# Kernel tuning notes

Measured on AMD Instinct MI355X. Metric: run time of the kernel, lower is better.

Reference implementation:

```python
import jax, jax.numpy as jnp
import numpy as np

N = 1024
H = 128

def setup_inputs() -> dict:
    key = jax.random.key(0)
    ks = jax.random.split(key, 16)
    s = 1.0 / np.sqrt(H)
    inp = {
        "h": jax.random.normal(ks[0], (N, H), jnp.float32),
        "x": jax.random.normal(ks[1], (N, 2), jnp.float32),
        "batch": jnp.zeros((N,), jnp.int64),
        # Linear params stored as [in, out]
        "Wq": jax.random.normal(ks[2], (H, H), jnp.float32) * s,
        "bq": jnp.zeros((H,), jnp.float32),
        "Wk": jax.random.normal(ks[3], (H, H), jnp.float32) * s,
        "bk": jnp.zeros((H,), jnp.float32),
        "Wv": jax.random.normal(ks[4], (H, H), jnp.float32) * s,
        "bv": jnp.zeros((H,), jnp.float32),
        "We1": jax.random.normal(ks[5], (2, H), jnp.float32) * (1.0 / np.sqrt(2.0)),
        "be1": jnp.zeros((H,), jnp.float32),
        "We2": jax.random.normal(ks[6], (H, H), jnp.float32) * s,
        "be2": jnp.zeros((H,), jnp.float32),
        "Wc": jax.random.normal(ks[7], (H, 1), jnp.float32) * s,
        "bc": jnp.zeros((1,), jnp.float32),
    }
    return inp

def reference(h, x, batch, Wq, bq, Wk, bk, Wv, bv, We1, be1, We2, be2, Wc, bc):
    hidden = h.shape[-1]
    # pairwise relative coordinates: [N, N, 2]
    rel_x = x[:, None, :] - x[None, :, :]
    # edge MLP: Linear(2->H) -> ReLU -> Linear(H->H), [N, N, H]
    edge_feat = jax.nn.relu(rel_x @ We1 + be1) @ We2 + be2
    # attention: scaled dot-product over all pairs
    q = h @ Wq + bq
    k = h @ Wk + bk
    v = h @ Wv + bv
    attn_score = (q @ k.T) / jnp.sqrt(jnp.asarray(hidden, h.dtype))  # [N, N]
    attn_weight = jax.nn.softmax(attn_score, axis=-1)
    agg_h = attn_weight @ v  # [N, H]
    # coordinate update: per-pair scalar gate times rel_x, attn-weighted sum over j
    gate = edge_feat @ Wc + bc                     # [N, N, 1]
    delta_x = jnp.sum(attn_weight[:, :, None] * gate * rel_x, axis=1)  # [N, 2]
    return (h + agg_h, x + delta_x)
```

## Files before the change

### kernel.cpp

```cpp
#include <hip/hip_runtime.h>
#include <math.h>

#define NN 1024
#define HH 128

typedef _Float16 h2 __attribute__((ext_vector_type(2)));
typedef _Float16 h4 __attribute__((ext_vector_type(4)));

__device__ inline float fdot2(h2 a, h2 b, float c) {
  return __builtin_amdgcn_fdot2(a, b, c, false);
}

__global__ __launch_bounds__(384) void qkv_kernel(
    const float* __restrict__ h,
    const float* __restrict__ Wq, const float* __restrict__ bq,
    const float* __restrict__ Wk, const float* __restrict__ bk,
    const float* __restrict__ Wv, const float* __restrict__ bv,
    const float* __restrict__ We2, const float* __restrict__ be2,
    const float* __restrict__ Wc, const float* __restrict__ bc,
    float* __restrict__ q, h2* __restrict__ kTp, h2* __restrict__ vp,
    float* __restrict__ Wc2, float* __restrict__ bc2) {
  const int t = threadIdx.x;

  if (blockIdx.x == 256) {
    if (t < HH) {
      float a = 0.f;
      for (int d = 0; d < HH; ++d) a = fmaf(We2[t * HH + d], Wc[d], a);
      Wc2[t] = a;
      if (t == 0) {
        float b = bc[0];
        for (int d = 0; d < HH; ++d) b = fmaf(be2[d], Wc[d], b);
        *bc2 = b;
      }
    }
    return;
  }

  __shared__ float4 hs4[HH];
  const int r0 = blockIdx.x * 4;
  if (t < HH) {
    hs4[t] = make_float4(h[(r0 + 0) * HH + t], h[(r0 + 1) * HH + t],
                         h[(r0 + 2) * HH + t], h[(r0 + 3) * HH + t]);
  }
  __syncthreads();

  const int mat = t >> 7;
  const int col = t & 127;
  const float* W = (mat == 0) ? Wq : (mat == 1) ? Wk : Wv;
  const float* B = (mat == 0) ? bq : (mat == 1) ? bk : bv;
  const float b = B[col];
  float a0 = b, a1 = b, a2 = b, a3 = b;
#pragma unroll 8
  for (int c = 0; c < HH; ++c) {
    float w = W[c * HH + col];
    float4 hv = hs4[c];
    a0 = fmaf(hv.x, w, a0);
    a1 = fmaf(hv.y, w, a1);
    a2 = fmaf(hv.z, w, a2);
    a3 = fmaf(hv.w, w, a3);
  }
  if (mat == 0) {
    q[(r0 + 0) * HH + col] = a0;
    q[(r0 + 1) * HH + col] = a1;
    q[(r0 + 2) * HH + col] = a2;
    q[(r0 + 3) * HH + col] = a3;
  } else if (mat == 1) {
    _Float16* kf = (_Float16*)kTp;
    const int base = ((col >> 1) * NN + r0) * 2 + (col & 1);
    kf[base + 0] = (_Float16)a0;
    kf[base + 2] = (_Float16)a1;
    kf[base + 4] = (_Float16)a2;
    kf[base + 6] = (_Float16)a3;
  } else {
    h2 v01, v23;
    v01.x = (_Float16)a0; v01.y = (_Float16)a1;
    v23.x = (_Float16)a2; v23.y = (_Float16)a3;
    h2* e = vp + ((r0 >> 1) * HH + col);
    e[0] = v01;
    e[HH] = v23;
  }
}

__global__ __launch_bounds__(512) void attn_kernel(
    const float* __restrict__ h, const float* __restrict__ x,
    const float* __restrict__ q, const h2* __restrict__ kTp,
    const h2* __restrict__ vp,
    const float* __restrict__ We1, const float* __restrict__ be1,
    const float* __restrict__ Wc2p, const float* __restrict__ bc2p,
    float* __restrict__ out) {
  __shared__ h4 qpx[HH / 2];
  __shared__ h4 wAB[HH / 2];
  __shared__ h4 wBC[HH / 2];
  __shared__ h4 wspi[NN / 2];
  __shared__ float xs[NN * 2];
  __shared__ float part[8][2][HH];
  __shared__ float red[6][8];

  const int i0 = blockIdx.x * 2, i1 = i0 + 1;
  const int tid = threadIdx.x;
  const int lane = tid & 63, wave = tid >> 6;

  if (tid < HH / 2) {
    const int u = tid;
    h4 a, b, c;
    a[0] = (_Float16)q[i0 * HH + 2 * u];
    a[1] = (_Float16)q[i0 * HH + 2 * u + 1];
    a[2] = (_Float16)q[i1 * HH + 2 * u];
    a[3] = (_Float16)q[i1 * HH + 2 * u + 1];
    qpx[u] = a;
    b[0] = (_Float16)We1[2 * u];
    b[1] = (_Float16)We1[2 * u + 1];
    b[2] = (_Float16)We1[HH + 2 * u];
    b[3] = (_Float16)We1[HH + 2 * u + 1];
    wAB[u] = b;
    c[0] = (_Float16)be1[2 * u];
    c[1] = (_Float16)be1[2 * u + 1];
    c[2] = (_Float16)Wc2p[2 * u];
    c[3] = (_Float16)Wc2p[2 * u + 1];
    wBC[u] = c;
  }
  for (int j = tid; j < NN * 2; j += 512) xs[j] = x[j];
  const float bc2 = *bc2p;
  __syncthreads();

  const float xi0x = xs[2 * i0], xi0y = xs[2 * i0 + 1];
  const float xi1x = xs[2 * i1], xi1y = xs[2 * i1 + 1];
  const int j0 = 2 * tid, j1 = j0 + 1;
  const float xj0x = xs[2 * j0], xj0y = xs[2 * j0 + 1];
  const float xj1x = xs[2 * j1], xj1y = xs[2 * j1 + 1];
  const float rx00 = xi0x - xj0x, ry00 = xi0y - xj0y;
  const float rx01 = xi0x - xj1x, ry01 = xi0y - xj1y;
  const float rx10 = xi1x - xj0x, ry10 = xi1y - xj0y;
  const float rx11 = xi1x - xj1x, ry11 = xi1y - xj1y;

  h2 RX00, RY00, RX01, RY01, RX10, RY10, RX11, RY11, Z2;
  RX00.x = RX00.y = (_Float16)rx00;  RY00.x = RY00.y = (_Float16)ry00;
  RX01.x = RX01.y = (_Float16)rx01;  RY01.x = RY01.y = (_Float16)ry01;
  RX10.x = RX10.y = (_Float16)rx10;  RY10.x = RY10.y = (_Float16)ry10;
  RX11.x = RX11.y = (_Float16)rx11;  RY11.x = RY11.y = (_Float16)ry11;
  Z2.x = Z2.y = (_Float16)0;

  float s00 = 0.f, s01 = 0.f, s10 = 0.f, s11 = 0.f;
  float g00 = bc2, g01 = bc2, g10 = bc2, g11 = bc2;
  const h4* kT4 = (const h4*)kTp;
#pragma unroll 4
  for (int u = 0; u < HH / 2; ++u) {
    h4 kk = kT4[u * (NN / 2) + tid];
    h4 qq = qpx[u];
    h4 ab = wAB[u];
    h4 bcv = wBC[u];
    h2 ka, kb, q0, q1, w0, w1, bb, cc;
    ka.x = kk[0]; ka.y = kk[1];
    kb.x = kk[2]; kb.y = kk[3];
    q0.x = qq[0]; q0.y = qq[1];
    q1.x = qq[2]; q1.y = qq[3];
    w0.x = ab[0]; w0.y = ab[1];
    w1.x = ab[2]; w1.y = ab[3];
    bb.x = bcv[0]; bb.y = bcv[1];
    cc.x = bcv[2]; cc.y = bcv[3];
    s00 = fdot2(q0, ka, s00);
    s01 = fdot2(q0, kb, s01);
    s10 = fdot2(q1, ka, s10);
    s11 = fdot2(q1, kb, s11);
    h2 t00 = RX00 * w0 + RY00 * w1 + bb;
    h2 t01 = RX01 * w0 + RY01 * w1 + bb;
    h2 t10 = RX10 * w0 + RY10 * w1 + bb;
    h2 t11 = RX11 * w0 + RY11 * w1 + bb;
    t00 = __builtin_elementwise_max(t00, Z2);
    t01 = __builtin_elementwise_max(t01, Z2);
    t10 = __builtin_elementwise_max(t10, Z2);
    t11 = __builtin_elementwise_max(t11, Z2);
    g00 = fdot2(t00, cc, g00);
    g01 = fdot2(t01, cc, g01);
    g10 = fdot2(t10, cc, g10);
    g11 = fdot2(t11, cc, g11);
  }
  const float scale = 0.08838834764831845f;
  const float e00 = __expf(s00 * scale), e01 = __expf(s01 * scale);
  const float e10 = __expf(s10 * scale), e11 = __expf(s11 * scale);
  {
    h4 w;
    w[0] = (_Float16)e00; w[1] = (_Float16)e01;
    w[2] = (_Float16)e10; w[3] = (_Float16)e11;
    wspi[tid] = w;
  }
  const float wg00 = e00 * g00, wg01 = e01 * g01;
  const float wg10 = e10 * g10, wg11 = e11 * g11;
  float l0 = e00 + e01, l1 = e10 + e11;
  float dx0 = fmaf(wg00, rx00, wg01 * rx01);
  float dy0 = fmaf(wg00, ry00, wg01 * ry01);
  float dx1 = fmaf(wg10, rx10, wg11 * rx11);
  float dy1 = fmaf(wg10, ry10, wg11 * ry11);
#pragma unroll
  for (int off = 32; off > 0; off >>= 1) {
    l0 += __shfl_down(l0, off);
    l1 += __shfl_down(l1, off);
    dx0 += __shfl_down(dx0, off);
    dy0 += __shfl_down(dy0, off);
    dx1 += __shfl_down(dx1, off);
    dy1 += __shfl_down(dy1, off);
  }
  if (lane == 0) {
    red[0][wave] = l0;  red[1][wave] = l1;
    red[2][wave] = dx0; red[3][wave] = dy0;
    red[4][wave] = dx1; red[5][wave] = dy1;
  }
  __syncthreads();
  float sum0 = 0.f, sum1 = 0.f;
#pragma unroll
  for (int w = 0; w < 8; ++w) { sum0 += red[0][w]; sum1 += red[1][w]; }
  const float inv0 = 1.f / sum0, inv1 = 1.f / sum1;

  if (tid == 0) {
    float DX0 = 0.f, DY0 = 0.f, DX1 = 0.f, DY1 = 0.f;
#pragma unroll
    for (int w = 0; w < 8; ++w) {
      DX0 += red[2][w]; DY0 += red[3][w];
      DX1 += red[4][w]; DY1 += red[5][w];
    }
    out[NN * HH + i0 * 2 + 0] = xi0x + DX0 * inv0;
    out[NN * HH + i0 * 2 + 1] = xi0y + DY0 * inv0;
    out[NN * HH + i1 * 2 + 0] = xi1x + DX1 * inv1;
    out[NN * HH + i1 * 2 + 1] = xi1y + DY1 * inv1;
  }

  {
    const int j2b = wave * 64;
    const h4* v4 = (const h4*)vp;
    float a0x = 0.f, a0y = 0.f, a1x = 0.f, a1y = 0.f;
#pragma unroll 4
    for (int jj = 0; jj < 64; ++jj) {
      const int j2 = j2b + jj;
      h4 vv = v4[j2 * 64 + lane];
      h4 wj = wspi[j2];
      h2 v0, v1, w0, w1;
      v0.x = vv[0]; v0.y = vv[1];
      v1.x = vv[2]; v1.y = vv[3];
      w0.x = wj[0]; w0.y = wj[1];
      w1.x = wj[2]; w1.y = wj[3];
      a0x = fdot2(w0, v0, a0x);
      a0y = fdot2(w0, v1, a0y);
      a1x = fdot2(w1, v0, a1x);
      a1y = fdot2(w1, v1, a1y);
    }
    part[wave][0][2 * lane] = a0x;
    part[wave][0][2 * lane + 1] = a0y;
    part[wave][1][2 * lane] = a1x;
    part[wave][1][2 * lane + 1] = a1y;
  }
  __syncthreads();
  if (tid < 256) {
    const int r = tid >> 7, c = tid & 127;
    float s = 0.f;
#pragma unroll
    for (int g = 0; g < 8; ++g) s += part[g][r][c];
    out[(i0 + r) * HH + c] = h[(i0 + r) * HH + c] + s * (r ? inv1 : inv0);
  }
}

extern "C" void kernel_launch(void* const* d_in, const int* in_sizes, int n_in,
                              void* d_out, int out_size, void* d_ws, size_t ws_size,
                              hipStream_t stream) {
  const float* h   = (const float*)d_in[0];
  const float* x   = (const float*)d_in[1];
  const float* Wq  = (const float*)d_in[3];
  const float* bq  = (const float*)d_in[4];
  const float* Wk  = (const float*)d_in[5];
  const float* bk  = (const float*)d_in[6];
  const float* Wv  = (const float*)d_in[7];
  const float* bv  = (const float*)d_in[8];
  const float* We1 = (const float*)d_in[9];
  const float* be1 = (const float*)d_in[10];
  const float* We2 = (const float*)d_in[11];
  const float* be2 = (const float*)d_in[12];
  const float* Wc  = (const float*)d_in[13];
  const float* bc  = (const float*)d_in[14];
  float* out = (float*)d_out;

  float* wsf = (float*)d_ws;
  float* q   = wsf;
  h2*   kTp  = (h2*)(wsf + NN * HH);
  h2*   vp   = kTp + (HH / 2) * NN;
  float* Wc2 = (float*)(vp + (NN / 2) * HH);
  float* bc2 = Wc2 + HH;

  qkv_kernel<<<257, 384, 0, stream>>>(h, Wq, bq, Wk, bk, Wv, bv, We2, be2, Wc,
                                      bc, q, kTp, vp, Wc2, bc2);
  attn_kernel<<<512, 512, 0, stream>>>(h, x, q, kTp, vp, We1, be1, Wc2, bc2,
                                       out);
}
```

Before: 110.6 us.

## Precompute per-node edge projections and widen K/V packed loads to h8

The first edge layer is linear in x_i - x_j, so it is rewritten as p_i - p_j with p = x @ We1. The qkv kernel computes p per node in a fourth wave group and interleaves it into the packed K buffer. The inner attention loop then does one subtract and a max instead of two multiply-adds plus a bias per pair. The softmax scale is folded into q, and V is repacked into 8-half vectors so the aggregation loop issues half as many wider loads. The cost is precision: the projection is rounded to fp16 before the subtraction, which may cause cancellation.

```diff
diff --git a/kernel.cpp b/kernel.cpp
--- a/kernel.cpp
+++ b/kernel.cpp
@@ -6,20 +6,23 @@
 
 typedef _Float16 h2 __attribute__((ext_vector_type(2)));
 typedef _Float16 h4 __attribute__((ext_vector_type(4)));
+typedef _Float16 h8 __attribute__((ext_vector_type(8)));
 
 __device__ inline float fdot2(h2 a, h2 b, float c) {
   return __builtin_amdgcn_fdot2(a, b, c, false);
 }
 
-__global__ __launch_bounds__(384) void qkv_kernel(
-    const float* __restrict__ h,
+__global__ __launch_bounds__(512) void qkv_kernel(
+    const float* __restrict__ h, const float* __restrict__ x,
     const float* __restrict__ Wq, const float* __restrict__ bq,
     const float* __restrict__ Wk, const float* __restrict__ bk,
     const float* __restrict__ Wv, const float* __restrict__ bv,
+    const float* __restrict__ We1,
     const float* __restrict__ We2, const float* __restrict__ be2,
     const float* __restrict__ Wc, const float* __restrict__ bc,
-    float* __restrict__ q, h2* __restrict__ kTp, h2* __restrict__ vp,
-    float* __restrict__ Wc2, float* __restrict__ bc2) {
+    float* __restrict__ q, _Float16* __restrict__ KP,
+    _Float16* __restrict__ VP, float* __restrict__ Wc2,
+    float* __restrict__ bc2) {
   const int t = threadIdx.x;
 
   if (blockIdx.x == 256) {
@@ -37,15 +40,29 @@
   }
 
   __shared__ float4 hs4[HH];
+  __shared__ float xsh[8];
   const int r0 = blockIdx.x * 4;
   if (t < HH) {
     hs4[t] = make_float4(h[(r0 + 0) * HH + t], h[(r0 + 1) * HH + t],
                          h[(r0 + 2) * HH + t], h[(r0 + 3) * HH + t]);
   }
+  if (t >= HH && t < HH + 8) xsh[t - HH] = x[r0 * 2 + (t - HH)];
   __syncthreads();
 
   const int mat = t >> 7;
   const int col = t & 127;
+
+  if (mat == 3) {
+    const float w0 = We1[col], w1 = We1[HH + col];
+    const int base = ((col >> 1) * (NN / 2) + (r0 >> 1)) * 8 + 4 + (col & 1);
+#pragma unroll
+    for (int rr = 0; rr < 4; ++rr) {
+      float p = fmaf(xsh[2 * rr], w0, xsh[2 * rr + 1] * w1);
+      KP[base + (rr >> 1) * 8 + (rr & 1) * 2] = (_Float16)p;
+    }
+    return;
+  }
+
   const float* W = (mat == 0) ? Wq : (mat == 1) ? Wk : Wv;
   const float* B = (mat == 0) ? bq : (mat == 1) ? bk : bv;
   const float b = B[col];
@@ -60,37 +77,34 @@
     a3 = fmaf(hv.w, w, a3);
   }
   if (mat == 0) {
-    q[(r0 + 0) * HH + col] = a0;
-    q[(r0 + 1) * HH + col] = a1;
-    q[(r0 + 2) * HH + col] = a2;
-    q[(r0 + 3) * HH + col] = a3;
+    const float scale = 0.08838834764831845f;
+    q[(r0 + 0) * HH + col] = a0 * scale;
+    q[(r0 + 1) * HH + col] = a1 * scale;
+    q[(r0 + 2) * HH + col] = a2 * scale;
+    q[(r0 + 3) * HH + col] = a3 * scale;
   } else if (mat == 1) {
-    _Float16* kf = (_Float16*)kTp;
-    const int base = ((col >> 1) * NN + r0) * 2 + (col & 1);
-    kf[base + 0] = (_Float16)a0;
-    kf[base + 2] = (_Float16)a1;
-    kf[base + 4] = (_Float16)a2;
-    kf[base + 6] = (_Float16)a3;
+    const int base = ((col >> 1) * (NN / 2) + (r0 >> 1)) * 8 + (col & 1);
+    KP[base + 0] = (_Float16)a0;
+    KP[base + 2] = (_Float16)a1;
+    KP[base + 8] = (_Float16)a2;
+    KP[base + 10] = (_Float16)a3;
   } else {
-    h2 v01, v23;
-    v01.x = (_Float16)a0; v01.y = (_Float16)a1;
-    v23.x = (_Float16)a2; v23.y = (_Float16)a3;
-    h2* e = vp + ((r0 >> 1) * HH + col);
-    e[0] = v01;
-    e[HH] = v23;
+    const int base = ((r0 >> 2) * (HH / 2) + (col >> 1)) * 8 + (col & 1) * 2;
+    VP[base + 0] = (_Float16)a0;
+    VP[base + 1] = (_Float16)a1;
+    VP[base + 4] = (_Float16)a2;
+    VP[base + 5] = (_Float16)a3;
   }
 }
 
 __global__ __launch_bounds__(512) void attn_kernel(
     const float* __restrict__ h, const float* __restrict__ x,
-    const float* __restrict__ q, const h2* __restrict__ kTp,
-    const h2* __restrict__ vp,
-    const float* __restrict__ We1, const float* __restrict__ be1,
+    const float* __restrict__ q, const h8* __restrict__ KP,
+    const h8* __restrict__ VP, const float* __restrict__ be1,
     const float* __restrict__ Wc2p, const float* __restrict__ bc2p,
     float* __restrict__ out) {
-  __shared__ h4 qpx[HH / 2];
-  __shared__ h4 wAB[HH / 2];
-  __shared__ h4 wBC[HH / 2];
+  __shared__ h8 qpp[HH / 2];
+  __shared__ h2 ccs[HH / 2];
   __shared__ h4 wspi[NN / 2];
   __shared__ float xs[NN * 2];
   __shared__ float part[8][2][HH];
@@ -102,22 +116,22 @@
 
   if (tid < HH / 2) {
     const int u = tid;
-    h4 a, b, c;
-    a[0] = (_Float16)q[i0 * HH + 2 * u];
-    a[1] = (_Float16)q[i0 * HH + 2 * u + 1];
-    a[2] = (_Float16)q[i1 * HH + 2 * u];
-    a[3] = (_Float16)q[i1 * HH + 2 * u + 1];
-    qpx[u] = a;
-    b[0] = (_Float16)We1[2 * u];
-    b[1] = (_Float16)We1[2 * u + 1];
-    b[2] = (_Float16)We1[HH + 2 * u];
-    b[3] = (_Float16)We1[HH + 2 * u + 1];
-    wAB[u] = b;
-    c[0] = (_Float16)be1[2 * u];
-    c[1] = (_Float16)be1[2 * u + 1];
-    c[2] = (_Float16)Wc2p[2 * u];
-    c[3] = (_Float16)Wc2p[2 * u + 1];
-    wBC[u] = c;
+    float2 qa = *(const float2*)(q + i0 * HH + 2 * u);
+    float2 qb = *(const float2*)(q + i1 * HH + 2 * u);
+    h8 kp = KP[u * (NN / 2) + (i0 >> 1)];
+    float2 b1 = *(const float2*)(be1 + 2 * u);
+    h8 a;
+    a[0] = (_Float16)qa.x; a[1] = (_Float16)qa.y;
+    a[2] = (_Float16)qb.x; a[3] = (_Float16)qb.y;
+    a[4] = (_Float16)((float)kp[4] + b1.x);
+    a[5] = (_Float16)((float)kp[5] + b1.y);
+    a[6] = (_Float16)((float)kp[6] + b1.x);
+    a[7] = (_Float16)((float)kp[7] + b1.y);
+    qpp[u] = a;
+    h2 c;
+    c.x = (_Float16)Wc2p[2 * u];
+    c.y = (_Float16)Wc2p[2 * u + 1];
+    ccs[u] = c;
   }
   for (int j = tid; j < NN * 2; j += 512) xs[j] = x[j];
   const float bc2 = *bc2p;
@@ -133,51 +147,41 @@
   const float rx10 = xi1x - xj0x, ry10 = xi1y - xj0y;
   const float rx11 = xi1x - xj1x, ry11 = xi1y - xj1y;
 
-  h2 RX00, RY00, RX01, RY01, RX10, RY10, RX11, RY11, Z2;
-  RX00.x = RX00.y = (_Float16)rx00;  RY00.x = RY00.y = (_Float16)ry00;
-  RX01.x = RX01.y = (_Float16)rx01;  RY01.x = RY01.y = (_Float16)ry01;
-  RX10.x = RX10.y = (_Float16)rx10;  RY10.x = RY10.y = (_Float16)ry10;
-  RX11.x = RX11.y = (_Float16)rx11;  RY11.x = RY11.y = (_Float16)ry11;
+  h2 Z2;
   Z2.x = Z2.y = (_Float16)0;
 
   float s00 = 0.f, s01 = 0.f, s10 = 0.f, s11 = 0.f;
   float g00 = bc2, g01 = bc2, g10 = bc2, g11 = bc2;
-  const h4* kT4 = (const h4*)kTp;
+  const h8* kptr = KP + tid;
 #pragma unroll 4
   for (int u = 0; u < HH / 2; ++u) {
-    h4 kk = kT4[u * (NN / 2) + tid];
-    h4 qq = qpx[u];
-    h4 ab = wAB[u];
-    h4 bcv = wBC[u];
-    h2 ka, kb, q0, q1, w0, w1, bb, cc;
-    ka.x = kk[0]; ka.y = kk[1];
-    kb.x = kk[2]; kb.y = kk[3];
-    q0.x = qq[0]; q0.y = qq[1];
-    q1.x = qq[2]; q1.y = qq[3];
-    w0.x = ab[0]; w0.y = ab[1];
-    w1.x = ab[2]; w1.y = ab[3];
-    bb.x = bcv[0]; bb.y = bcv[1];
-    cc.x = bcv[2]; cc.y = bcv[3];
+    h8 kp = kptr[u * (NN / 2)];
+    h8 qp = qpp[u];
+    h2 cc = ccs[u];
+    h2 ka, kb, pj0, pj1, q0, q1, pi0, pi1;
+    ka.x = kp[0]; ka.y = kp[1];
+    kb.x = kp[2]; kb.y = kp[3];
+    pj0.x = kp[4]; pj0.y = kp[5];
+    pj1.x = kp[6]; pj1.y = kp[7];
+    q0.x = qp[0]; q0.y = qp[1];
+    q1.x = qp[2]; q1.y = qp[3];
+    pi0.x = qp[4]; pi0.y = qp[5];
+    pi1.x = qp[6]; pi1.y = qp[7];
     s00 = fdot2(q0, ka, s00);
     s01 = fdot2(q0, kb, s01);
     s10 = fdot2(q1, ka, s10);
     s11 = fdot2(q1, kb, s11);
-    h2 t00 = RX00 * w0 + RY00 * w1 + bb;
-    h2 t01 = RX01 * w0 + RY01 * w1 + bb;
-    h2 t10 = RX10 * w0 + RY10 * w1 + bb;
-    h2 t11 = RX11 * w0 + RY11 * w1 + bb;
-    t00 = __builtin_elementwise_max(t00, Z2);
-    t01 = __builtin_elementwise_max(t01, Z2);
-    t10 = __builtin_elementwise_max(t10, Z2);
-    t11 = __builtin_elementwise_max(t11, Z2);
+    h2 t00 = __builtin_elementwise_max(pi0 - pj0, Z2);
+    h2 t01 = __builtin_elementwise_max(pi0 - pj1, Z2);
+    h2 t10 = __builtin_elementwise_max(pi1 - pj0, Z2);
+    h2 t11 = __builtin_elementwise_max(pi1 - pj1, Z2);
     g00 = fdot2(t00, cc, g00);
     g01 = fdot2(t01, cc, g01);
     g10 = fdot2(t10, cc, g10);
     g11 = fdot2(t11, cc, g11);
   }
-  const float scale = 0.08838834764831845f;
-  const float e00 = __expf(s00 * scale), e01 = __expf(s01 * scale);
-  const float e10 = __expf(s10 * scale), e11 = __expf(s11 * scale);
+  const float e00 = __expf(s00), e01 = __expf(s01);
+  const float e10 = __expf(s10), e11 = __expf(s11);
   {
     h4 w;
     w[0] = (_Float16)e00; w[1] = (_Float16)e01;
@@ -225,23 +229,31 @@
   }
 
   {
-    const int j2b = wave * 64;
-    const h4* v4 = (const h4*)vp;
+    const int j4b = wave * 32;
+    const h8* wsp8 = (const h8*)wspi;
     float a0x = 0.f, a0y = 0.f, a1x = 0.f, a1y = 0.f;
 #pragma unroll 4
-    for (int jj = 0; jj < 64; ++jj) {
-      const int j2 = j2b + jj;
-      h4 vv = v4[j2 * 64 + lane];
-      h4 wj = wspi[j2];
-      h2 v0, v1, w0, w1;
-      v0.x = vv[0]; v0.y = vv[1];
-      v1.x = vv[2]; v1.y = vv[3];
-      w0.x = wj[0]; w0.y = wj[1];
-      w1.x = wj[2]; w1.y = wj[3];
-      a0x = fdot2(w0, v0, a0x);
-      a0y = fdot2(w0, v1, a0y);
-      a1x = fdot2(w1, v0, a1x);
-      a1y = fdot2(w1, v1, a1y);
+    for (int jj = 0; jj < 32; ++jj) {
+      const int j4 = j4b + jj;
+      h8 vv = VP[j4 * (HH / 2) + lane];
+      h8 wj = wsp8[j4];
+      h2 w0a, w1a, w0b, w1b, v0a, v1a, v0b, v1b;
+      w0a.x = wj[0]; w0a.y = wj[1];
+      w1a.x = wj[2]; w1a.y = wj[3];
+      w0b.x = wj[4]; w0b.y = wj[5];
+      w1b.x = wj[6]; w1b.y = wj[7];
+      v0a.x = vv[0]; v0a.y = vv[1];
+      v1a.x = vv[2]; v1a.y = vv[3];
+      v0b.x = vv[4]; v0b.y = vv[5];
+      v1b.x = vv[6]; v1b.y = vv[7];
+      a0x = fdot2(w0a, v0a, a0x);
+      a0x = fdot2(w0b, v0b, a0x);
+      a0y = fdot2(w0a, v1a, a0y);
+      a0y = fdot2(w0b, v1b, a0y);
+      a1x = fdot2(w1a, v0a, a1x);
+      a1x = fdot2(w1b, v0b, a1x);
+      a1y = fdot2(w1a, v1a, a1y);
+      a1y = fdot2(w1b, v1b, a1y);
     }
     part[wave][0][2 * lane] = a0x;
     part[wave][0][2 * lane + 1] = a0y;
@@ -278,14 +290,14 @@
   float* out = (float*)d_out;
 
   float* wsf = (float*)d_ws;
-  float* q   = wsf;
-  h2*   kTp  = (h2*)(wsf + NN * HH);
-  h2*   vp   = kTp + (HH / 2) * NN;
-  float* Wc2 = (float*)(vp + (NN / 2) * HH);
+  float* q = wsf;
+  _Float16* KP = (_Float16*)(wsf + NN * HH);
+  _Float16* VP = KP + (HH / 2) * (NN / 2) * 8;
+  float* Wc2 = (float*)(VP + (NN / 4) * (HH / 2) * 8);
   float* bc2 = Wc2 + HH;
 
-  qkv_kernel<<<257, 384, 0, stream>>>(h, Wq, bq, Wk, bk, Wv, bv, We2, be2, Wc,
-                                      bc, q, kTp, vp, Wc2, bc2);
-  attn_kernel<<<512, 512, 0, stream>>>(h, x, q, kTp, vp, We1, be1, Wc2, bc2,
-                                       out);
+  qkv_kernel<<<257, 512, 0, stream>>>(h, x, Wq, bq, Wk, bk, Wv, bv, We1, We2,
+                                      be2, Wc, bc, q, KP, VP, Wc2, bc2);
+  attn_kernel<<<512, 512, 0, stream>>>(h, x, q, (const h8*)KP, (const h8*)VP,
+                                       be1, Wc2, bc2, out);
 }
```

Result: faster. 106.2 us (-4.0%).
